# Kernel optimization log

Measured on AMD Instinct MI355X. Metric: run time of the kernel, lower is better.

Reference implementation:

```python
import jax, jax.numpy as jnp
import numpy as np

N = 12000       # nodes (Hi-C bins, max_num_nodes)
F_IN = 16       # number_genomic_annotations
HID = 4 * F_IN  # conv1 out = 64
NCLUST = 100    # n_clust
E = 384000      # edges (avg degree 32)


def setup_inputs() -> dict:
    key = jax.random.key(0)
    ks = jax.random.split(key, 8)
    x = jax.random.normal(ks[0], (N, F_IN), dtype=jnp.float32)
    edge_index = jax.random.randint(ks[1], (2, E), 0, N)
    edge_attr = jax.random.uniform(ks[2], (E,), dtype=jnp.float32)
    s1 = 1.0 / np.sqrt(F_IN)
    W1_rel = jax.random.uniform(ks[3], (HID, F_IN), minval=-s1, maxval=s1, dtype=jnp.float32)
    W1_root = jax.random.uniform(ks[4], (HID, F_IN), minval=-s1, maxval=s1, dtype=jnp.float32)
    b1 = jnp.zeros((HID,), jnp.float32)
    s2 = 1.0 / np.sqrt(HID)
    W2_rel = jax.random.uniform(ks[5], (NCLUST, HID), minval=-s2, maxval=s2, dtype=jnp.float32)
    W2_root = jax.random.uniform(ks[6], (NCLUST, HID), minval=-s2, maxval=s2, dtype=jnp.float32)
    b2 = jnp.zeros((NCLUST,), jnp.float32)
    return dict(x=x, edge_index=edge_index, edge_attr=edge_attr,
                W1_rel=W1_rel, W1_root=W1_root, b1=b1,
                W2_rel=W2_rel, W2_root=W2_root, b2=b2)


def _graph_conv(x, src, dst, ew, W_rel, W_root, b):
    # PyG GraphConv (aggr='add'): out = lin_rel(sum_j e_ji * x_j) + lin_root(x)
    msg = x[src] * ew[:, None]                       # [E, F]
    aggr = jax.ops.segment_sum(msg, dst, num_segments=N)  # [N, F]
    return aggr @ W_rel.T + b + x @ W_root.T


def reference(x, edge_index, edge_attr, W1_rel, W1_root, b1, W2_rel, W2_root, b2):
    src, dst = edge_index[0], edge_index[1]
    h = _graph_conv(x, src, dst, edge_attr, W1_rel, W1_root, b1)
    h = jax.nn.relu(h)  # dropout is identity in eval mode
    s_out = _graph_conv(h, src, dst, edge_attr, W2_rel, W2_root, b2)  # [N, NCLUST]

    # to_dense_adj (duplicate edges summed)
    adj = jnp.zeros((N, N), x.dtype).at[src, dst].add(edge_attr)  # [N, N]

    # dense_mincut_pool with S = x (as in the original forward), k = F_IN
    s_mc = jax.nn.softmax(x, axis=-1)      # [N, F_IN]
    as_ = adj @ s_mc                        # [N, F_IN]
    out_adj = s_mc.T @ as_                  # [F_IN, F_IN]
    mincut_num = jnp.trace(out_adj)
    d_flat = adj.sum(-1)                    # [N] degree
    mincut_den = jnp.einsum('ik,i,ik->', s_mc, d_flat, s_mc)  # trace(S^T D S)
    mc = -(mincut_num / mincut_den)

    ss = s_mc.T @ s_mc                      # [F_IN, F_IN]
    i_k = jnp.eye(F_IN, dtype=ss.dtype)
    o = jnp.linalg.norm(ss / jnp.linalg.norm(ss) - i_k / jnp.linalg.norm(i_k))

    return jax.nn.softmax(s_out, axis=-1), mc, o
```

## Files before the change

kernel.cpp:

```cpp
#include <hip/hip_runtime.h>
#include <math.h>

#define N_NODES 12000
#define F_INN 16
#define HIDD 64
#define NCLUST 100
#define NEDGE 384000
#define NBLK_N 47
#define CAP 96
#define EPT 4
#define NBLK_E 375
#define NBLK_F1 (N_NODES / 4)

#define OFF_COUNT   0
#define OFF_SCAL    12000
#define ZERO_ELEMS  12002
#define OFF_SSPART  12004
#define OFF_NORM2   24036
#define OFF_W2TREL  36036
#define OFF_W2TROOT 42436
#define OFF_SMC     48836
#define OFF_H       240836
#define OFF_SRCW    1008836

__global__ void zero_kernel(int* __restrict__ ws) {
    int i = blockIdx.x * 256 + threadIdx.x;
    if (i < ZERO_ELEMS) ws[i] = 0;
}

__global__ void phase0_kernel(const float* __restrict__ x, const int* __restrict__ ei,
                              const float* __restrict__ ew, float* __restrict__ smc,
                              float* __restrict__ norm2, int* __restrict__ count,
                              int2* __restrict__ srcw, const float* __restrict__ W2_rel,
                              const float* __restrict__ W2_root, float* __restrict__ w2t_rel,
                              float* __restrict__ w2t_root) {
    __shared__ float fl[6400];
    int t = threadIdx.x;
    int b = blockIdx.x;
    if (b < NBLK_N) {
        int i = b * 256 + t;
        if (i >= N_NODES) return;
        const float4* xr = (const float4*)(x + i * 16);
        float4 r0 = xr[0], r1 = xr[1], r2 = xr[2], r3 = xr[3];
        float v[16] = {r0.x, r0.y, r0.z, r0.w, r1.x, r1.y, r1.z, r1.w,
                       r2.x, r2.y, r2.z, r2.w, r3.x, r3.y, r3.z, r3.w};
        float m = v[0];
#pragma unroll
        for (int k = 1; k < 16; ++k) m = fmaxf(m, v[k]);
        float s = 0.f;
#pragma unroll
        for (int k = 0; k < 16; ++k) { v[k] = __expf(v[k] - m); s += v[k]; }
        float inv = 1.f / s;
        float n2 = 0.f;
#pragma unroll
        for (int k = 0; k < 16; ++k) { v[k] *= inv; n2 += v[k] * v[k]; }
        float4* so = (float4*)(smc + i * 16);
        so[0] = make_float4(v[0], v[1], v[2], v[3]);
        so[1] = make_float4(v[4], v[5], v[6], v[7]);
        so[2] = make_float4(v[8], v[9], v[10], v[11]);
        so[3] = make_float4(v[12], v[13], v[14], v[15]);
        norm2[i] = n2;
    } else if (b < NBLK_N + NBLK_E) {
        int tid = (b - NBLK_N) * 256 + t;
        int e0 = tid * EPT;
        int4 sv = *(const int4*)(ei + e0);
        int4 dv = *(const int4*)(ei + NEDGE + e0);
        float4 wv = *(const float4*)(ew + e0);
        int s[EPT] = {sv.x, sv.y, sv.z, sv.w};
        int d[EPT] = {dv.x, dv.y, dv.z, dv.w};
        float w[EPT] = {wv.x, wv.y, wv.z, wv.w};
        int pos[EPT];
#pragma unroll
        for (int i = 0; i < EPT; ++i) pos[i] = atomicAdd(&count[d[i]], 1);
#pragma unroll
        for (int i = 0; i < EPT; ++i)
            srcw[d[i] * CAP + pos[i]] = make_int2(s[i], __float_as_int(w[i]));
    } else {
        const float* src = (b == NBLK_N + NBLK_E) ? W2_rel : W2_root;
        float* dst = (b == NBLK_N + NBLK_E) ? w2t_rel : w2t_root;
        for (int i = t; i < 6400; i += 256) fl[i] = src[i];
        __syncthreads();
        for (int j = t; j < 6400; j += 256) {
            int kk = j / 100, cl = j - kk * 100;
            dst[j] = fl[cl * 64 + kk];
        }
    }
}

__global__ void fused1_pass2_kernel(const float* __restrict__ x, const int2* __restrict__ srcw,
                                    const int* __restrict__ count, const float* __restrict__ W1_rel,
                                    const float* __restrict__ W1_root, const float* __restrict__ b1,
                                    float* __restrict__ h, const float* __restrict__ smc,
                                    float* __restrict__ sspart, const int* __restrict__ ei,
                                    const float* __restrict__ ew, const float* __restrict__ norm2,
                                    float* __restrict__ scal) {
    __shared__ float shm[4352];
    int t = threadIdx.x;
    int b = blockIdx.x;
    if (b < NBLK_F1) {
        float* wrelT  = shm;
        float* wrootT = shm + 1024;
        float* b1s    = shm + 2048;
        float* aggr   = shm + 2112;
        float* xs     = shm + 2176;
        for (int idx = t; idx < 1024; idx += 256) {
            int f = idx >> 4, k = idx & 15;
            wrelT[(k << 6) + f]  = W1_rel[idx];
            wrootT[(k << 6) + f] = W1_root[idx];
        }
        if (t < 64) b1s[t] = b1[t];
        int w = t >> 6, lane = t & 63;
        int j2 = lane >> 2;
        int q  = lane & 3;
        int n = b * 4 + w;
        int len = count[n];
        const int2* bucket = srcw + n * CAP;
        float4 acc4 = make_float4(0.f, 0.f, 0.f, 0.f);
        int k = 0;
        for (; k + 31 < len; k += 32) {
            int2 pa = bucket[k + j2];
            int2 pb = bucket[k + 16 + j2];
            float4 va = *(const float4*)(x + pa.x * 16 + q * 4);
            float4 vb = *(const float4*)(x + pb.x * 16 + q * 4);
            float wa = __int_as_float(pa.y), wb = __int_as_float(pb.y);
            acc4.x = fmaf(va.x, wa, acc4.x); acc4.y = fmaf(va.y, wa, acc4.y);
            acc4.z = fmaf(va.z, wa, acc4.z); acc4.w = fmaf(va.w, wa, acc4.w);
            acc4.x = fmaf(vb.x, wb, acc4.x); acc4.y = fmaf(vb.y, wb, acc4.y);
            acc4.z = fmaf(vb.z, wb, acc4.z); acc4.w = fmaf(vb.w, wb, acc4.w);
        }
        for (; k < len; k += 16) {
            if (k + j2 < len) {
                int2 p = bucket[k + j2];
                float4 v = *(const float4*)(x + p.x * 16 + q * 4);
                float wt = __int_as_float(p.y);
                acc4.x = fmaf(v.x, wt, acc4.x); acc4.y = fmaf(v.y, wt, acc4.y);
                acc4.z = fmaf(v.z, wt, acc4.z); acc4.w = fmaf(v.w, wt, acc4.w);
            }
        }
        acc4.x += __shfl_xor(acc4.x, 4);  acc4.y += __shfl_xor(acc4.y, 4);
        acc4.z += __shfl_xor(acc4.z, 4);  acc4.w += __shfl_xor(acc4.w, 4);
        acc4.x += __shfl_xor(acc4.x, 8);  acc4.y += __shfl_xor(acc4.y, 8);
        acc4.z += __shfl_xor(acc4.z, 8);  acc4.w += __shfl_xor(acc4.w, 8);
        acc4.x += __shfl_xor(acc4.x, 16); acc4.y += __shfl_xor(acc4.y, 16);
        acc4.z += __shfl_xor(acc4.z, 16); acc4.w += __shfl_xor(acc4.w, 16);
        acc4.x += __shfl_xor(acc4.x, 32); acc4.y += __shfl_xor(acc4.y, 32);
        acc4.z += __shfl_xor(acc4.z, 32); acc4.w += __shfl_xor(acc4.w, 32);
        if (j2 == 0) *(float4*)(aggr + w * 16 + q * 4) = acc4;
        if (lane < 16) xs[w * 16 + lane] = x[n * 16 + lane];
        __syncthreads();
        float o = b1s[lane];
#pragma unroll
        for (int kk = 0; kk < 16; ++kk)
            o = fmaf(aggr[w * 16 + kk], wrelT[(kk << 6) + lane],
                     fmaf(xs[w * 16 + kk], wrootT[(kk << 6) + lane], o));
        h[n * 64 + lane] = fmaxf(o, 0.f);
    } else if (b < NBLK_F1 + NBLK_N) {
        int bb = b - NBLK_F1;
        float* rows = shm;
        int n = bb * 256 + t;
        float* rp = rows + t * 17;
        if (n < N_NODES) {
            const float4* sr = (const float4*)(smc + n * 16);
            float4 a0 = sr[0], a1 = sr[1], a2v = sr[2], a3 = sr[3];
            rp[0] = a0.x;  rp[1] = a0.y;  rp[2] = a0.z;  rp[3] = a0.w;
            rp[4] = a1.x;  rp[5] = a1.y;  rp[6] = a1.z;  rp[7] = a1.w;
            rp[8] = a2v.x; rp[9] = a2v.y; rp[10] = a2v.z; rp[11] = a2v.w;
            rp[12] = a3.x; rp[13] = a3.y; rp[14] = a3.z; rp[15] = a3.w;
        } else {
#pragma unroll
            for (int k = 0; k < 16; ++k) rp[k] = 0.f;
        }
        __syncthreads();
        int a = t & 15, bq = t >> 4;
        float accs = 0.f;
#pragma unroll 4
        for (int r = 0; r < 256; ++r)
            accs = fmaf(rows[r * 17 + a], rows[r * 17 + bq], accs);
        sspart[bb * 256 + t] = accs;
    } else {
        int tid = (b - NBLK_F1 - NBLK_N) * 256 + t;
        int e0 = tid * EPT;
        int4 sv = *(const int4*)(ei + e0);
        int4 dv = *(const int4*)(ei + NEDGE + e0);
        float4 wv = *(const float4*)(ew + e0);
        int s[EPT] = {sv.x, sv.y, sv.z, sv.w};
        int d[EPT] = {dv.x, dv.y, dv.z, dv.w};
        float w[EPT] = {wv.x, wv.y, wv.z, wv.w};
        float np = 0.f, dp = 0.f;
#pragma unroll
        for (int i = 0; i < EPT; ++i) {
            const float4* ps = (const float4*)(smc + s[i] * 16);
            const float4* pd = (const float4*)(smc + d[i] * 16);
            float4 s0 = ps[0], s1 = ps[1], s2 = ps[2], s3 = ps[3];
            float4 d0 = pd[0], d1 = pd[1], d2 = pd[2], d3 = pd[3];
            float dot = s0.x * d0.x + s0.y * d0.y + s0.z * d0.z + s0.w * d0.w +
                        s1.x * d1.x + s1.y * d1.y + s1.z * d1.z + s1.w * d1.w +
                        s2.x * d2.x + s2.y * d2.y + s2.z * d2.z + s2.w * d2.w +
                        s3.x * d3.x + s3.y * d3.y + s3.z * d3.z + s3.w * d3.w;
            np = fmaf(w[i], dot, np);
            dp = fmaf(w[i], norm2[s[i]], dp);
        }
        float* redn = shm;
        float* redd = shm + 256;
        redn[t] = np;
        redd[t] = dp;
        __syncthreads();
        for (int s2 = 128; s2 > 0; s2 >>= 1) {
            if (t < s2) { redn[t] += redn[t + s2]; redd[t] += redd[t + s2]; }
            __syncthreads();
        }
        if (t == 0) {
            atomicAdd(&scal[0], redn[0]);
            atomicAdd(&scal[1], redd[0]);
        }
    }
}

__global__ void fused2_finalize_kernel(const float* __restrict__ h, const int2* __restrict__ srcw,
                                       const int* __restrict__ count,
                                       const float* __restrict__ w2t_rel,
                                       const float* __restrict__ w2t_root,
                                       const float* __restrict__ b2, float* __restrict__ out,
                                       const float* __restrict__ sspart,
                                       const float* __restrict__ scal) {
    __shared__ float shm[1328];
    int t = threadIdx.x;
    int b = blockIdx.x;
    if (b < NBLK_F1) {
        float* a2   = shm;
        float* hrow = shm + 256;
        float* logits = shm + 512;
        float* part = shm + 928;
        int nn = t >> 6;
        int c = t & 63;
        int eslot = c >> 4;
        int q = c & 15;
        int n = b * 4 + nn;
        int len = count[n];
        const int2* bucket = srcw + n * CAP;
        float4 acc4 = make_float4(0.f, 0.f, 0.f, 0.f);
        int k = 0;
        for (; k + 31 < len; k += 32) {
            int2 pa = bucket[k + eslot];
            int2 pb = bucket[k + 4 + eslot];
            int2 pc = bucket[k + 8 + eslot];
            int2 pd = bucket[k + 12 + eslot];
            int2 pe = bucket[k + 16 + eslot];
            int2 pf = bucket[k + 20 + eslot];
            int2 pg = bucket[k + 24 + eslot];
            int2 ph = bucket[k + 28 + eslot];
            float4 va = *(const float4*)(h + pa.x * 64 + q * 4);
            float4 vb = *(const float4*)(h + pb.x * 64 + q * 4);
            float4 vc = *(const float4*)(h + pc.x * 64 + q * 4);
            float4 vd = *(const float4*)(h + pd.x * 64 + q * 4);
            float4 ve = *(const float4*)(h + pe.x * 64 + q * 4);
            float4 vf = *(const float4*)(h + pf.x * 64 + q * 4);
            float4 vg = *(const float4*)(h + pg.x * 64 + q * 4);
            float4 vh = *(const float4*)(h + ph.x * 64 + q * 4);
            float wa = __int_as_float(pa.y), wb = __int_as_float(pb.y);
            float wc = __int_as_float(pc.y), wd = __int_as_float(pd.y);
            float we = __int_as_float(pe.y), wf = __int_as_float(pf.y);
            float wg = __int_as_float(pg.y), wh = __int_as_float(ph.y);
            acc4.x = fmaf(va.x, wa, acc4.x); acc4.y = fmaf(va.y, wa, acc4.y);
            acc4.z = fmaf(va.z, wa, acc4.z); acc4.w = fmaf(va.w, wa, acc4.w);
            acc4.x = fmaf(vb.x, wb, acc4.x); acc4.y = fmaf(vb.y, wb, acc4.y);
            acc4.z = fmaf(vb.z, wb, acc4.z); acc4.w = fmaf(vb.w, wb, acc4.w);
            acc4.x = fmaf(vc.x, wc, acc4.x); acc4.y = fmaf(vc.y, wc, acc4.y);
            acc4.z = fmaf(vc.z, wc, acc4.z); acc4.w = fmaf(vc.w, wc, acc4.w);
            acc4.x = fmaf(vd.x, wd, acc4.x); acc4.y = fmaf(vd.y, wd, acc4.y);
            acc4.z = fmaf(vd.z, wd, acc4.z); acc4.w = fmaf(vd.w, wd, acc4.w);
            acc4.x = fmaf(ve.x, we, acc4.x); acc4.y = fmaf(ve.y, we, acc4.y);
            acc4.z = fmaf(ve.z, we, acc4.z); acc4.w = fmaf(ve.w, we, acc4.w);
            acc4.x = fmaf(vf.x, wf, acc4.x); acc4.y = fmaf(vf.y, wf, acc4.y);
            acc4.z = fmaf(vf.z, wf, acc4.z); acc4.w = fmaf(vf.w, wf, acc4.w);
            acc4.x = fmaf(vg.x, wg, acc4.x); acc4.y = fmaf(vg.y, wg, acc4.y);
            acc4.z = fmaf(vg.z, wg, acc4.z); acc4.w = fmaf(vg.w, wg, acc4.w);
            acc4.x = fmaf(vh.x, wh, acc4.x); acc4.y = fmaf(vh.y, wh, acc4.y);
            acc4.z = fmaf(vh.z, wh, acc4.z); acc4.w = fmaf(vh.w, wh, acc4.w);
        }
        for (; k < len; k += 4) {
            if (k + eslot < len) {
                int2 p = bucket[k + eslot];
                float4 v = *(const float4*)(h + p.x * 64 + q * 4);
                float wt = __int_as_float(p.y);
                acc4.x = fmaf(v.x, wt, acc4.x); acc4.y = fmaf(v.y, wt, acc4.y);
                acc4.z = fmaf(v.z, wt, acc4.z); acc4.w = fmaf(v.w, wt, acc4.w);
            }
        }
        acc4.x += __shfl_xor(acc4.x, 16); acc4.y += __shfl_xor(acc4.y, 16);
        acc4.z += __shfl_xor(acc4.z, 16); acc4.w += __shfl_xor(acc4.w, 16);
        acc4.x += __shfl_xor(acc4.x, 32); acc4.y += __shfl_xor(acc4.y, 32);
        acc4.z += __shfl_xor(acc4.z, 32); acc4.w += __shfl_xor(acc4.w, 32);
        if (eslot == 0) *(float4*)(a2 + nn * 64 + q * 4) = acc4;
        hrow[nn * 64 + c] = h[n * 64 + c];
        __syncthreads();
        int half = t >> 7, c2 = t & 127;
        float p0 = 0.f, p1 = 0.f, p2 = 0.f, p3 = 0.f;
        if (c2 < NCLUST) {
            int kbase = half << 5;
#pragma unroll 8
            for (int kk = kbase; kk < kbase + 32; ++kk) {
                float wr = w2t_rel[kk * 100 + c2];
                float wo = w2t_root[kk * 100 + c2];
                p0 = fmaf(a2[0 * 64 + kk], wr, fmaf(hrow[0 * 64 + kk], wo, p0));
                p1 = fmaf(a2[1 * 64 + kk], wr, fmaf(hrow[1 * 64 + kk], wo, p1));
                p2 = fmaf(a2[2 * 64 + kk], wr, fmaf(hrow[2 * 64 + kk], wo, p2));
                p3 = fmaf(a2[3 * 64 + kk], wr, fmaf(hrow[3 * 64 + kk], wo, p3));
            }
            if (half == 1) {
                part[0 * 100 + c2] = p0;
                part[1 * 100 + c2] = p1;
                part[2 * 100 + c2] = p2;
                part[3 * 100 + c2] = p3;
            }
        }
        __syncthreads();
        if (half == 0 && c2 < NCLUST) {
            float bb = b2[c2];
            logits[0 * 104 + c2] = bb + p0 + part[0 * 100 + c2];
            logits[1 * 104 + c2] = bb + p1 + part[1 * 100 + c2];
            logits[2 * 104 + c2] = bb + p2 + part[2 * 100 + c2];
            logits[3 * 104 + c2] = bb + p3 + part[3 * 100 + c2];
        }
        __syncthreads();
        float v0 = logits[nn * 104 + c];
        float v1 = (c < NCLUST - 64) ? logits[nn * 104 + 64 + c] : -INFINITY;
        float m = fmaxf(v0, v1);
#pragma unroll
        for (int off = 32; off > 0; off >>= 1) m = fmaxf(m, __shfl_xor(m, off));
        float e0 = __expf(v0 - m);
        float e1 = (c < NCLUST - 64) ? __expf(v1 - m) : 0.f;
        float s = e0 + e1;
#pragma unroll
        for (int off = 32; off > 0; off >>= 1) s += __shfl_xor(s, off);
        float inv = 1.f / s;
        out[n * NCLUST + c] = e0 * inv;
        if (c < NCLUST - 64) out[n * NCLUST + 64 + c] = e1 * inv;
    } else {
        float* red = shm;
        float sv = 0.f;
        for (int bb = 0; bb < NBLK_N; ++bb) sv += sspart[bb * 256 + t];
        red[t] = sv * sv;
        __syncthreads();
        for (int s = 128; s > 0; s >>= 1) {
            if (t < s) red[t] += red[t + s];
            __syncthreads();
        }
        float ssnorm = sqrtf(red[0]);
        __syncthreads();
        float diff = sv / ssnorm - ((t % 17 == 0) ? 0.25f : 0.f);
        red[t] = diff * diff;
        __syncthreads();
        for (int s = 128; s > 0; s >>= 1) {
            if (t < s) red[t] += red[t + s];
            __syncthreads();
        }
        if (t == 0) {
            out[N_NODES * NCLUST + 0] = -(scal[0] / scal[1]);
            out[N_NODES * NCLUST + 1] = sqrtf(red[0]);
        }
    }
}

extern "C" void kernel_launch(void* const* d_in, const int* in_sizes, int n_in,
                              void* d_out, int out_size, void* d_ws, size_t ws_size,
                              hipStream_t stream) {
    const float* x       = (const float*)d_in[0];
    const int*   ei      = (const int*)d_in[1];
    const float* ew      = (const float*)d_in[2];
    const float* W1_rel  = (const float*)d_in[3];
    const float* W1_root = (const float*)d_in[4];
    const float* b1      = (const float*)d_in[5];
    const float* W2_rel  = (const float*)d_in[6];
    const float* W2_root = (const float*)d_in[7];
    const float* b2      = (const float*)d_in[8];
    float* out = (float*)d_out;
    int*   wsi = (int*)d_ws;

    int*   count   = wsi + OFF_COUNT;
    float* scal    = (float*)(wsi + OFF_SCAL);
    float* sspart  = (float*)(wsi + OFF_SSPART);
    float* norm2   = (float*)(wsi + OFF_NORM2);
    float* w2trel  = (float*)(wsi + OFF_W2TREL);
    float* w2troot = (float*)(wsi + OFF_W2TROOT);
    float* smc     = (float*)(wsi + OFF_SMC);
    float* h       = (float*)(wsi + OFF_H);
    int2*  srcw    = (int2*)(wsi + OFF_SRCW);

    zero_kernel<<<(ZERO_ELEMS + 255) / 256, 256, 0, stream>>>(wsi);
    phase0_kernel<<<NBLK_N + NBLK_E + 2, 256, 0, stream>>>(x, ei, ew, smc, norm2, count, srcw,
                                                           W2_rel, W2_root, w2trel, w2troot);
    fused1_pass2_kernel<<<NBLK_F1 + NBLK_N + NBLK_E, 256, 0, stream>>>(
        x, srcw, count, W1_rel, W1_root, b1, h, smc, sspart, ei, ew, norm2, scal);
    fused2_finalize_kernel<<<NBLK_F1 + 1, 256, 0, stream>>>(h, srcw, count, w2trel, w2troot,
                                                            b2, out, sspart, scal);
}
```

Measured before the change: 104.1 us.

## Process eight nodes per block in layer-2 kernel with shared-memory W2_rel and nontemporal stores

The layer-2 aggregation/projection kernel now uses 512-thread blocks covering 8 nodes each. It stages W2_rel^T (25.6 KB) and b2 in shared memory, and each 128-thread group computes full 64-wide dot products for two nodes, which removes the split-K partial-sum pass and one barrier. Edge bucket writes and h writes become nontemporal stores. The trade-off is a per-block 6400-float shared load and higher LDS use, which may limit occupancy.

Result: no change. 102.9 us (-1.1%).

```diff
diff --git a/kernel.cpp b/kernel.cpp
--- a/kernel.cpp
+++ b/kernel.cpp
@@ -11,6 +11,7 @@
 #define EPT 4
 #define NBLK_E 375
 #define NBLK_F1 (N_NODES / 4)
+#define NBLK_F2 (N_NODES / 8)
 
 #define OFF_COUNT   0
 #define OFF_SCAL    12000
@@ -73,8 +74,11 @@
 #pragma unroll
         for (int i = 0; i < EPT; ++i) pos[i] = atomicAdd(&count[d[i]], 1);
 #pragma unroll
-        for (int i = 0; i < EPT; ++i)
-            srcw[d[i] * CAP + pos[i]] = make_int2(s[i], __float_as_int(w[i]));
+        for (int i = 0; i < EPT; ++i) {
+            unsigned long long pv = ((unsigned long long)(unsigned)__float_as_int(w[i]) << 32) |
+                                    (unsigned)s[i];
+            __builtin_nontemporal_store(pv, (unsigned long long*)&srcw[d[i] * CAP + pos[i]]);
+        }
     } else {
         const float* src = (b == NBLK_N + NBLK_E) ? W2_rel : W2_root;
         float* dst = (b == NBLK_N + NBLK_E) ? w2t_rel : w2t_root;
@@ -153,7 +157,7 @@
         for (int kk = 0; kk < 16; ++kk)
             o = fmaf(aggr[w * 16 + kk], wrelT[(kk << 6) + lane],
                      fmaf(xs[w * 16 + kk], wrootT[(kk << 6) + lane], o));
-        h[n * 64 + lane] = fmaxf(o, 0.f);
+        __builtin_nontemporal_store(fmaxf(o, 0.f), &h[n * 64 + lane]);
     } else if (b < NBLK_F1 + NBLK_N) {
         int bb = b - NBLK_F1;
         float* rows = shm;
@@ -216,26 +220,25 @@
     }
 }
 
-__global__ void fused2_finalize_kernel(const float* __restrict__ h, const int2* __restrict__ srcw,
-                                       const int* __restrict__ count,
-                                       const float* __restrict__ w2t_rel,
-                                       const float* __restrict__ w2t_root,
-                                       const float* __restrict__ b2, float* __restrict__ out,
-                                       const float* __restrict__ sspart,
-                                       const float* __restrict__ scal) {
-    __shared__ float shm[1328];
+__global__ __launch_bounds__(512) void fused2_finalize_kernel(
+    const float* __restrict__ h, const int2* __restrict__ srcw, const int* __restrict__ count,
+    const float* __restrict__ w2t_rel, const float* __restrict__ w2t_root,
+    const float* __restrict__ b2, float* __restrict__ out, const float* __restrict__ sspart,
+    const float* __restrict__ scal) {
+    __shared__ float wsrel[6400];
+    __shared__ float a2[8][64], hrow[8][64];
+    __shared__ float logits[8][104];
+    __shared__ float b2s[104];
     int t = threadIdx.x;
     int b = blockIdx.x;
-    if (b < NBLK_F1) {
-        float* a2   = shm;
-        float* hrow = shm + 256;
-        float* logits = shm + 512;
-        float* part = shm + 928;
+    if (b < NBLK_F2) {
+        for (int i = t; i < 6400; i += 512) wsrel[i] = w2t_rel[i];
+        if (t < NCLUST) b2s[t] = b2[t];
         int nn = t >> 6;
         int c = t & 63;
         int eslot = c >> 4;
         int q = c & 15;
-        int n = b * 4 + nn;
+        int n = b * 8 + nn;
         int len = count[n];
         const int2* bucket = srcw + n * CAP;
         float4 acc4 = make_float4(0.f, 0.f, 0.f, 0.f);
@@ -291,40 +294,26 @@
         acc4.z += __shfl_xor(acc4.z, 16); acc4.w += __shfl_xor(acc4.w, 16);
         acc4.x += __shfl_xor(acc4.x, 32); acc4.y += __shfl_xor(acc4.y, 32);
         acc4.z += __shfl_xor(acc4.z, 32); acc4.w += __shfl_xor(acc4.w, 32);
-        if (eslot == 0) *(float4*)(a2 + nn * 64 + q * 4) = acc4;
-        hrow[nn * 64 + c] = h[n * 64 + c];
-        __syncthreads();
-        int half = t >> 7, c2 = t & 127;
-        float p0 = 0.f, p1 = 0.f, p2 = 0.f, p3 = 0.f;
+        if (eslot == 0) *(float4*)(&a2[nn][q * 4]) = acc4;
+        hrow[nn][c] = h[n * 64 + c];
+        __syncthreads();
+        int g = t >> 7, c2 = t & 127;
         if (c2 < NCLUST) {
-            int kbase = half << 5;
+            int na = 2 * g, nb2 = 2 * g + 1;
+            float s0 = b2s[c2], s1 = s0;
 #pragma unroll 8
-            for (int kk = kbase; kk < kbase + 32; ++kk) {
-                float wr = w2t_rel[kk * 100 + c2];
+            for (int kk = 0; kk < 64; ++kk) {
+                float wr = wsrel[kk * 100 + c2];
                 float wo = w2t_root[kk * 100 + c2];
-                p0 = fmaf(a2[0 * 64 + kk], wr, fmaf(hrow[0 * 64 + kk], wo, p0));
-                p1 = fmaf(a2[1 * 64 + kk], wr, fmaf(hrow[1 * 64 + kk], wo, p1));
-                p2 = fmaf(a2[2 * 64 + kk], wr, fmaf(hrow[2 * 64 + kk], wo, p2));
-                p3 = fmaf(a2[3 * 64 + kk], wr, fmaf(hrow[3 * 64 + kk], wo, p3));
+                s0 = fmaf(a2[na][kk], wr, fmaf(hrow[na][kk], wo, s0));
+                s1 = fmaf(a2[nb2][kk], wr, fmaf(hrow[nb2][kk], wo, s1));
             }
-            if (half == 1) {
-                part[0 * 100 + c2] = p0;
-                part[1 * 100 + c2] = p1;
-                part[2 * 100 + c2] = p2;
-                part[3 * 100 + c2] = p3;
-            }
-        }
-        __syncthreads();
-        if (half == 0 && c2 < NCLUST) {
-            float bb = b2[c2];
-            logits[0 * 104 + c2] = bb + p0 + part[0 * 100 + c2];
-            logits[1 * 104 + c2] = bb + p1 + part[1 * 100 + c2];
-            logits[2 * 104 + c2] = bb + p2 + part[2 * 100 + c2];
-            logits[3 * 104 + c2] = bb + p3 + part[3 * 100 + c2];
-        }
-        __syncthreads();
-        float v0 = logits[nn * 104 + c];
-        float v1 = (c < NCLUST - 64) ? logits[nn * 104 + 64 + c] : -INFINITY;
+            logits[na][c2] = s0;
+            logits[nb2][c2] = s1;
+        }
+        __syncthreads();
+        float v0 = logits[nn][c];
+        float v1 = (c < NCLUST - 64) ? logits[nn][64 + c] : -INFINITY;
         float m = fmaxf(v0, v1);
 #pragma unroll
         for (int off = 32; off > 0; off >>= 1) m = fmaxf(m, __shfl_xor(m, off));
@@ -337,21 +326,22 @@
         out[n * NCLUST + c] = e0 * inv;
         if (c < NCLUST - 64) out[n * NCLUST + 64 + c] = e1 * inv;
     } else {
-        float* red = shm;
+        float* red = wsrel;
         float sv = 0.f;
-        for (int bb = 0; bb < NBLK_N; ++bb) sv += sspart[bb * 256 + t];
+        if (t < 256)
+            for (int bb = 0; bb < NBLK_N; ++bb) sv += sspart[bb * 256 + t];
         red[t] = sv * sv;
         __syncthreads();
-        for (int s = 128; s > 0; s >>= 1) {
+        for (int s = 256; s > 0; s >>= 1) {
             if (t < s) red[t] += red[t + s];
             __syncthreads();
         }
         float ssnorm = sqrtf(red[0]);
         __syncthreads();
-        float diff = sv / ssnorm - ((t % 17 == 0) ? 0.25f : 0.f);
+        float diff = (t < 256) ? (sv / ssnorm - ((t % 17 == 0) ? 0.25f : 0.f)) : 0.f;
         red[t] = diff * diff;
         __syncthreads();
-        for (int s = 128; s > 0; s >>= 1) {
+        for (int s = 256; s > 0; s >>= 1) {
             if (t < s) red[t] += red[t + s];
             __syncthreads();
         }
@@ -392,6 +382,6 @@
                                                            W2_rel, W2_root, w2trel, w2troot);
     fused1_pass2_kernel<<<NBLK_F1 + NBLK_N + NBLK_E, 256, 0, stream>>>(
         x, srcw, count, W1_rel, W1_root, b1, h, smc, sspart, ei, ew, norm2, scal);
-    fused2_finalize_kernel<<<NBLK_F1 + 1, 256, 0, stream>>>(h, srcw, count, w2trel, w2troot,
+    fused2_finalize_kernel<<<NBLK_F2 + 1, 512, 0, stream>>>(h, srcw, count, w2trel, w2troot,
                                                             b2, out, sspart, scal);
 }
```
